# Optimization experiments

Hardware: AMD Instinct MI355X
Metric: run time of the kernel (lower is better)

## Reference

```python
import jax, jax.numpy as jnp
import numpy as np
import math

B, S, E, H = 2, 2048, 1024, 16
D = E // H  # head_dim = 64
WINDOW = 512
EPS = 1e-5


def _layernorm(x, gamma, beta):
    mu = jnp.mean(x, axis=-1, keepdims=True)
    var = jnp.var(x, axis=-1, keepdims=True)
    return (x - mu) * jax.lax.rsqrt(var + EPS) * gamma + beta


def setup_inputs() -> dict:
    key = jax.random.key(0)
    ks = jax.random.split(key, 5)
    return {
        "x": jax.random.normal(ks[0], (B, S, E), jnp.float32),
        "W_qkv": jax.random.normal(ks[1], (E, 3 * E), jnp.float32) * (E ** -0.5),
        "b_qkv": jax.random.normal(ks[2], (3 * E,), jnp.float32) * 0.02,
        "q_gamma": jnp.ones((D,), jnp.float32),
        "q_beta": jnp.zeros((D,), jnp.float32),
        "k_gamma": jnp.ones((D,), jnp.float32),
        "k_beta": jnp.zeros((D,), jnp.float32),
        "W_out": jax.random.normal(ks[3], (E, E), jnp.float32) * (E ** -0.5),
        "b_out": jax.random.normal(ks[4], (E,), jnp.float32) * 0.02,
    }


def reference(x, W_qkv, b_qkv, q_gamma, q_beta, k_gamma, k_beta, W_out, b_out):
    b, s, e = x.shape
    # fused QKV projection -> (3, B, H, S, D)
    qkv = (x @ W_qkv + b_qkv).reshape(b, s, 3, H, D).transpose(2, 0, 3, 1, 4)
    q, k, v = qkv[0], qkv[1], qkv[2]
    # qk_norm: LayerNorm over head_dim
    q = _layernorm(q, q_gamma, q_beta)
    k = _layernorm(k, k_gamma, k_beta)
    scores = jnp.einsum("bhqd,bhkd->bhqk", q, k) / math.sqrt(D)
    # causal + sliding-window mask (True = masked out)
    row = jnp.arange(s)[:, None]
    col = jnp.arange(s)[None, :]
    masked = (col > row) | (row - col >= WINDOW)  # sliding window subsumes causal
    scores = jnp.where(masked[None, None], -jnp.inf, scores)
    attn = jax.nn.softmax(scores, axis=-1)
    out = jnp.einsum("bhqk,bhkd->bhqd", attn, v)  # (B,H,S,D)
    out = out.transpose(0, 2, 1, 3).reshape(b, s, e)
    return out @ W_out + b_out
```

## Files before the change

### kernel.cpp

```cpp
#include <hip/hip_runtime.h>
#include <stdint.h>

typedef uint16_t u16;
typedef __attribute__((ext_vector_type(8))) short short8;
typedef __attribute__((ext_vector_type(4))) float f32x4;

#define DEV static __device__ __forceinline__

DEV u16 f2bf(float f) {
  uint32_t u = __float_as_uint(f);
  return (u16)((u + 0x7fffu + ((u >> 16) & 1u)) >> 16);
}
DEV float bf2f(u16 h) { return __uint_as_float(((uint32_t)h) << 16); }

DEV void gload16(const void* g, void* l) {
  __builtin_amdgcn_global_load_lds(
      (const __attribute__((address_space(1))) void*)g,
      (__attribute__((address_space(3))) void*)l, 16, 0, 0);
}

__global__ void k_cast4(const float* __restrict__ in, u16* __restrict__ out, int n4) {
  int i = blockIdx.x * blockDim.x + threadIdx.x;
  if (i >= n4) return;
  float4 v = ((const float4*)in)[i];
  uint2 p;
  p.x = (uint32_t)f2bf(v.x) | ((uint32_t)f2bf(v.y) << 16);
  p.y = (uint32_t)f2bf(v.z) | ((uint32_t)f2bf(v.w) << 16);
  ((uint2*)out)[i] = p;
}

__global__ void k_tcast(const float* __restrict__ Wm, u16* __restrict__ Wt, int K, int N) {
  __shared__ u16 t[64][65];
  int n0 = blockIdx.x * 64, k0 = blockIdx.y * 64;
  int tid = threadIdx.x;
#pragma unroll
  for (int i = 0; i < 16; ++i) {
    int idx = tid + i * 256, r = idx >> 6, c = idx & 63;
    t[r][c] = f2bf(Wm[(size_t)(k0 + r) * N + n0 + c]);
  }
  __syncthreads();
#pragma unroll
  for (int i = 0; i < 16; ++i) {
    int idx = tid + i * 256, r = idx >> 6, c = idx & 63;
    Wt[(size_t)(n0 + r) * K + k0 + c] = t[c][r];
  }
}

__global__ __launch_bounds__(256) void k_gemmqkv(
    const u16* __restrict__ A, const u16* __restrict__ Bt,
    const float* __restrict__ bias,
    const float* __restrict__ qg, const float* __restrict__ qb,
    const float* __restrict__ kg, const float* __restrict__ kb,
    u16* __restrict__ Qn, u16* __restrict__ Kn, u16* __restrict__ Vt) {
  const int K = 1024, N = 3072;
  __shared__ __attribute__((aligned(16))) u16 S[2][2][128 * 64];
  int bid = blockIdx.x;
  int ntn = N >> 7;
  int cpx = gridDim.x >> 3;
  int wg = (bid & 7) * cpx + (bid >> 3);
  int my = wg / ntn, nx = wg - my * ntn;
  int m0 = my * 128, n0 = nx * 128;
  int tid = threadIdx.x, lane = tid & 63, w = tid >> 6;
  int wr = (w >> 1) * 64, wc = (w & 1) * 64;
  int lr = lane & 15, lg = lane >> 4;
  int rsw = (lr & 7) << 3;
  int srow = tid >> 3;
  int scb = ((tid & 7) ^ ((tid >> 3) & 7)) * 8;
  f32x4 acc[4][4];
#pragma unroll
  for (int i = 0; i < 4; ++i)
#pragma unroll
    for (int j = 0; j < 4; ++j) acc[i][j] = (f32x4){0.f, 0.f, 0.f, 0.f};

  int nk = K >> 6;

#define STGQ(buf, kt)                                                                   \
  do {                                                                                  \
    gload16(A + (size_t)(m0 + srow) * K + (kt) * 64 + scb, &S[buf][0][tid * 8]);        \
    gload16(A + (size_t)(m0 + 32 + srow) * K + (kt) * 64 + scb, &S[buf][0][2048 + tid * 8]);  \
    gload16(A + (size_t)(m0 + 64 + srow) * K + (kt) * 64 + scb, &S[buf][0][4096 + tid * 8]);  \
    gload16(A + (size_t)(m0 + 96 + srow) * K + (kt) * 64 + scb, &S[buf][0][6144 + tid * 8]);  \
    gload16(Bt + (size_t)(n0 + srow) * K + (kt) * 64 + scb, &S[buf][1][tid * 8]);       \
    gload16(Bt + (size_t)(n0 + 32 + srow) * K + (kt) * 64 + scb, &S[buf][1][2048 + tid * 8]); \
    gload16(Bt + (size_t)(n0 + 64 + srow) * K + (kt) * 64 + scb, &S[buf][1][4096 + tid * 8]); \
    gload16(Bt + (size_t)(n0 + 96 + srow) * K + (kt) * 64 + scb, &S[buf][1][6144 + tid * 8]); \
  } while (0)

  STGQ(0, 0);
  asm volatile("s_waitcnt vmcnt(0)" ::: "memory");
  __syncthreads();

  for (int t = 0; t < nk; ++t) {
    int cur = t & 1;
    if (t + 1 < nk) STGQ(cur ^ 1, t + 1);
#pragma unroll
    for (int ks = 0; ks < 2; ++ks) {
      short8 af[4], bf[4];
#pragma unroll
      for (int mi = 0; mi < 4; ++mi)
        af[mi] = *(const short8*)&S[cur][0][((wr + mi * 16 + lr) * 64 + ks * 32 + lg * 8) ^ rsw];
#pragma unroll
      for (int ni = 0; ni < 4; ++ni)
        bf[ni] = *(const short8*)&S[cur][1][((wc + ni * 16 + lr) * 64 + ks * 32 + lg * 8) ^ rsw];
      __builtin_amdgcn_s_setprio(1);
#pragma unroll
      for (int mi = 0; mi < 4; ++mi)
#pragma unroll
        for (int ni = 0; ni < 4; ++ni)
          acc[mi][ni] = __builtin_amdgcn_mfma_f32_16x16x32_bf16(af[mi], bf[ni], acc[mi][ni], 0, 0, 0);
      __builtin_amdgcn_s_setprio(0);
    }
    asm volatile("s_waitcnt vmcnt(0)" ::: "memory");
    __syncthreads();
  }
#undef STGQ

  int rg = lg * 4;
  int sec = n0 >> 10;
  int hh = ((n0 + wc) >> 6) & 15;
  int b = m0 >> 11;
  int s0 = m0 & 2047;

  if (sec < 2) {
    const float* gp = sec ? kg : qg;
    const float* bp = sec ? kb : qb;
    float scl = sec ? 1.f : (0.125f * 1.44269504f);
    u16* op = sec ? Kn : Qn;
    float gv[4], bev[4], bb[4];
#pragma unroll
    for (int ni = 0; ni < 4; ++ni) {
      int d = ni * 16 + lr;
      gv[ni] = gp[d];
      bev[ni] = bp[d];
      bb[ni] = bias[n0 + wc + d];
    }
    size_t hb = (size_t)(b * 16 + hh) * 2048 * 64;
#pragma unroll
    for (int mi = 0; mi < 4; ++mi) {
      float a[4][4], ps[4], ps2[4];
#pragma unroll
      for (int ni = 0; ni < 4; ++ni)
#pragma unroll
        for (int j = 0; j < 4; ++j) a[ni][j] = acc[mi][ni][j] + bb[ni];
#pragma unroll
      for (int j = 0; j < 4; ++j) {
        ps[j] = a[0][j] + a[1][j] + a[2][j] + a[3][j];
        ps2[j] = a[0][j] * a[0][j] + a[1][j] * a[1][j] + a[2][j] * a[2][j] + a[3][j] * a[3][j];
      }
#pragma unroll
      for (int m = 1; m < 16; m <<= 1)
#pragma unroll
        for (int j = 0; j < 4; ++j) {
          ps[j] += __shfl_xor(ps[j], m, 64);
          ps2[j] += __shfl_xor(ps2[j], m, 64);
        }
#pragma unroll
      for (int j = 0; j < 4; ++j) {
        float mean = ps[j] * (1.f / 64);
        float var = ps2[j] * (1.f / 64) - mean * mean;
        float r = rsqrtf(var + 1e-5f);
        int row = s0 + wr + mi * 16 + rg + j;
        size_t base = hb + (size_t)row * 64;
#pragma unroll
        for (int ni = 0; ni < 4; ++ni) {
          float v = ((a[ni][j] - mean) * r * gv[ni] + bev[ni]) * scl;
          op[base + ni * 16 + lr] = f2bf(v);
        }
      }
    }
  } else {
    u16* vbase = Vt + (size_t)(b * 16 + hh) * 64 * 2048;
#pragma unroll
    for (int ni = 0; ni < 4; ++ni) {
      int d = ni * 16 + lr;
      float bb = bias[n0 + wc + d];
#pragma unroll
      for (int mi = 0; mi < 4; ++mi) {
        int row0 = s0 + wr + mi * 16 + rg;
        uint2 pk;
        pk.x = (uint32_t)f2bf(acc[mi][ni][0] + bb) | ((uint32_t)f2bf(acc[mi][ni][1] + bb) << 16);
        pk.y = (uint32_t)f2bf(acc[mi][ni][2] + bb) | ((uint32_t)f2bf(acc[mi][ni][3] + bb) << 16);
        *(uint2*)(vbase + (size_t)d * 2048 + row0) = pk;
      }
    }
  }
}

template <int OUT_BF16>
__global__ __launch_bounds__(256) void k_gemm4(
    const u16* __restrict__ A, const u16* __restrict__ Bt,
    const float* __restrict__ bias, void* __restrict__ Cout,
    int M, int N, int K) {
  __shared__ __attribute__((aligned(16))) u16 S[2][2][128 * 64];
  int bid = blockIdx.x;
  int ntn = N >> 7;
  int cpx = gridDim.x >> 3;
  int wg = (bid & 7) * cpx + (bid >> 3);
  int my = wg / ntn, nx = wg - my * ntn;
  int m0 = my * 128, n0 = nx * 128;
  int tid = threadIdx.x, lane = tid & 63, w = tid >> 6;
  int wr = (w >> 1) * 64, wc = (w & 1) * 64;
  int lr = lane & 15, lg = lane >> 4;
  int rsw = (lr & 7) << 3;
  int srow = tid >> 3;
  int scb = ((tid & 7) ^ ((tid >> 3) & 7)) * 8;
  f32x4 acc[4][4];
#pragma unroll
  for (int i = 0; i < 4; ++i)
#pragma unroll
    for (int j = 0; j < 4; ++j) acc[i][j] = (f32x4){0.f, 0.f, 0.f, 0.f};

  int nk = K >> 6;

#define STG4(buf, kt)                                                                   \
  do {                                                                                  \
    gload16(A + (size_t)(m0 + srow) * K + (kt) * 64 + scb, &S[buf][0][tid * 8]);        \
    gload16(A + (size_t)(m0 + 32 + srow) * K + (kt) * 64 + scb, &S[buf][0][2048 + tid * 8]);  \
    gload16(A + (size_t)(m0 + 64 + srow) * K + (kt) * 64 + scb, &S[buf][0][4096 + tid * 8]);  \
    gload16(A + (size_t)(m0 + 96 + srow) * K + (kt) * 64 + scb, &S[buf][0][6144 + tid * 8]);  \
    gload16(Bt + (size_t)(n0 + srow) * K + (kt) * 64 + scb, &S[buf][1][tid * 8]);       \
    gload16(Bt + (size_t)(n0 + 32 + srow) * K + (kt) * 64 + scb, &S[buf][1][2048 + tid * 8]); \
    gload16(Bt + (size_t)(n0 + 64 + srow) * K + (kt) * 64 + scb, &S[buf][1][4096 + tid * 8]); \
    gload16(Bt + (size_t)(n0 + 96 + srow) * K + (kt) * 64 + scb, &S[buf][1][6144 + tid * 8]); \
  } while (0)

  STG4(0, 0);
  asm volatile("s_waitcnt vmcnt(0)" ::: "memory");
  __syncthreads();

  for (int t = 0; t < nk; ++t) {
    int cur = t & 1;
    if (t + 1 < nk) STG4(cur ^ 1, t + 1);
#pragma unroll
    for (int ks = 0; ks < 2; ++ks) {
      short8 af[4], bf[4];
#pragma unroll
      for (int mi = 0; mi < 4; ++mi)
        af[mi] = *(const short8*)&S[cur][0][((wr + mi * 16 + lr) * 64 + ks * 32 + lg * 8) ^ rsw];
#pragma unroll
      for (int ni = 0; ni < 4; ++ni)
        bf[ni] = *(const short8*)&S[cur][1][((wc + ni * 16 + lr) * 64 + ks * 32 + lg * 8) ^ rsw];
      __builtin_amdgcn_s_setprio(1);
#pragma unroll
      for (int mi = 0; mi < 4; ++mi)
#pragma unroll
        for (int ni = 0; ni < 4; ++ni)
          acc[mi][ni] = __builtin_amdgcn_mfma_f32_16x16x32_bf16(af[mi], bf[ni], acc[mi][ni], 0, 0, 0);
      __builtin_amdgcn_s_setprio(0);
    }
    asm volatile("s_waitcnt vmcnt(0)" ::: "memory");
    __syncthreads();
  }
#undef STG4

  int rg = lg * 4;
#pragma unroll
  for (int mi = 0; mi < 4; ++mi) {
#pragma unroll
    for (int ni = 0; ni < 4; ++ni) {
      int col = n0 + wc + ni * 16 + lr;
      float bv = bias[col];
#pragma unroll
      for (int j = 0; j < 4; ++j) {
        int row = m0 + wr + mi * 16 + rg + j;
        float o = acc[mi][ni][j] + bv;
        if (OUT_BF16) ((u16*)Cout)[(size_t)row * N + col] = f2bf(o);
        else ((float*)Cout)[(size_t)row * N + col] = o;
      }
    }
  }
}

__global__ __launch_bounds__(256) void k_attn6(
    const u16* __restrict__ Qn, const u16* __restrict__ Kn,
    const u16* __restrict__ Vt, u16* __restrict__ attb) {
  __shared__ __attribute__((aligned(16))) u16 KL[2][4096];
  __shared__ __attribute__((aligned(16))) u16 VL[2][4096];
  __shared__ __attribute__((aligned(16))) u16 Pl[4][16 * 72];
  int bid = blockIdx.x;
  int xcd = bid & 7, idx = bid >> 3;
  int bh = xcd * 4 + (idx & 3);
  int qt = 31 - (idx >> 2);
  int q0 = qt * 64;
  int tid = threadIdx.x, lane = tid & 63, w = tid >> 6;
  int ln15 = lane & 15, lg = lane >> 4;
  int qlo = q0 + w * 16;
  const u16* Qh = Qn + (size_t)bh * (2048 * 64);
  const u16* Kh = Kn + (size_t)bh * (2048 * 64);
  const u16* Vh = Vt + (size_t)bh * (64 * 2048);
  int rsw = (ln15 & 7) << 3;
  int srow = tid >> 3;
  int scb = ((tid & 7) ^ ((tid >> 3) & 7)) * 8;

  short8 qf[2];
#pragma unroll
  for (int h2 = 0; h2 < 2; ++h2)
    qf[h2] = *(const short8*)(Qh + (size_t)(qlo + ln15) * 64 + h2 * 32 + lg * 8);

  f32x4 oacc[4];
#pragma unroll
  for (int dt = 0; dt < 4; ++dt) oacc[dt] = (f32x4){0.f, 0.f, 0.f, 0.f};
  float lwp[4] = {0.f, 0.f, 0.f, 0.f};

  int t0 = q0 >= 512 ? (q0 - 511) >> 6 : 0;
  int t1 = (q0 + 63) >> 6;

#define STAGE_A6(buf, kt)                                                              \
  do {                                                                                 \
    const u16* Kt_ = Kh + (size_t)(kt) * 4096;                                         \
    gload16(Kt_ + (size_t)srow * 64 + scb, &KL[buf][tid * 8]);                         \
    gload16(Kt_ + (size_t)(srow + 32) * 64 + scb, &KL[buf][2048 + tid * 8]);           \
    const u16* Vt_ = Vh + (size_t)(kt) * 64;                                           \
    gload16(Vt_ + (size_t)srow * 2048 + scb, &VL[buf][tid * 8]);                       \
    gload16(Vt_ + (size_t)(srow + 32) * 2048 + scb, &VL[buf][2048 + tid * 8]);         \
  } while (0)

  STAGE_A6(0, t0);
  asm volatile("s_waitcnt vmcnt(0)" ::: "memory");
  __syncthreads();

  for (int t = t0; t <= t1; ++t) {
    int cur = (t - t0) & 1;
    if (t + 1 <= t1) STAGE_A6(cur ^ 1, t + 1);
    int kt6 = t * 64;
    if (kt6 <= qlo + 15 && kt6 + 63 >= qlo - 511) {
      short8 kf[4][2];
#pragma unroll
      for (int c = 0; c < 4; ++c)
#pragma unroll
        for (int h2 = 0; h2 < 2; ++h2)
          kf[c][h2] = *(const short8*)&KL[cur][((c * 16 + ln15) * 64 + h2 * 32 + lg * 8) ^ rsw];
      f32x4 sf[4];
      __builtin_amdgcn_s_setprio(1);
#pragma unroll
      for (int c = 0; c < 4; ++c) {
        f32x4 z = (f32x4){0.f, 0.f, 0.f, 0.f};
        z = __builtin_amdgcn_mfma_f32_16x16x32_bf16(qf[0], kf[c][0], z, 0, 0, 0);
        sf[c] = __builtin_amdgcn_mfma_f32_16x16x32_bf16(qf[1], kf[c][1], z, 0, 0, 0);
      }
      __builtin_amdgcn_s_setprio(0);
      bool interior = (kt6 + 63 <= qlo) && (kt6 >= qlo - 496);
      if (interior) {
#pragma unroll
        for (int c = 0; c < 4; ++c)
#pragma unroll
          for (int j = 0; j < 4; ++j) {
            float p = __builtin_amdgcn_exp2f(sf[c][j]);
            sf[c][j] = p;
            lwp[j] += p;
          }
      } else {
#pragma unroll
        for (int c = 0; c < 4; ++c) {
          int kk = kt6 + c * 16 + ln15;
#pragma unroll
          for (int j = 0; j < 4; ++j) {
            int q = qlo + lg * 4 + j;
            bool msk = (kk > q) || ((q - kk) >= 512);
            float p = __builtin_amdgcn_exp2f(msk ? -1e30f : sf[c][j]);
            sf[c][j] = p;
            lwp[j] += p;
          }
        }
      }
#pragma unroll
      for (int c = 0; c < 4; ++c)
#pragma unroll
        for (int j = 0; j < 4; ++j) {
          uint32_t u = __float_as_uint(sf[c][j]);
          Pl[w][(lg * 4 + j) * 72 + c * 16 + ln15] = (u16)((u + 0x8000u) >> 16);
        }
      short8 vf[4][2];
#pragma unroll
      for (int dt = 0; dt < 4; ++dt)
#pragma unroll
        for (int h2 = 0; h2 < 2; ++h2)
          vf[dt][h2] = *(const short8*)&VL[cur][((dt * 16 + ln15) * 64 + h2 * 32 + lg * 8) ^ rsw];
      __builtin_amdgcn_s_setprio(1);
#pragma unroll
      for (int h2 = 0; h2 < 2; ++h2) {
        short8 pf = *(const short8*)&Pl[w][ln15 * 72 + h2 * 32 + lg * 8];
#pragma unroll
        for (int dt = 0; dt < 4; ++dt)
          oacc[dt] = __builtin_amdgcn_mfma_f32_16x16x32_bf16(pf, vf[dt][h2], oacc[dt], 0, 0, 0);
      }
      __builtin_amdgcn_s_setprio(0);
    }
    asm volatile("s_waitcnt vmcnt(0)" ::: "memory");
    __syncthreads();
  }
#undef STAGE_A6

  int b = bh >> 4, hh = bh & 15;
#pragma unroll
  for (int j = 0; j < 4; ++j) {
    float rs = lwp[j];
#pragma unroll
    for (int m = 8; m > 0; m >>= 1) rs += __shfl_xor(rs, m, 64);
    float inv = rs > 0.f ? 1.f / rs : 0.f;
    int row = b * 2048 + qlo + lg * 4 + j;
#pragma unroll
    for (int dt = 0; dt < 4; ++dt)
      attb[(size_t)row * 1024 + hh * 64 + dt * 16 + ln15] = f2bf(oacc[dt][j] * inv);
  }
}

extern "C" void kernel_launch(void* const* d_in, const int* in_sizes, int n_in,
                              void* d_out, int out_size, void* d_ws, size_t ws_size,
                              hipStream_t stream) {
  const float* x = (const float*)d_in[0];
  const float* Wqkv = (const float*)d_in[1];
  const float* bqkv = (const float*)d_in[2];
  const float* qg = (const float*)d_in[3];
  const float* qb = (const float*)d_in[4];
  const float* kg = (const float*)d_in[5];
  const float* kb = (const float*)d_in[6];
  const float* Wout = (const float*)d_in[7];
  const float* bout = (const float*)d_in[8];
  float* out = (float*)d_out;

  char* ws = (char*)d_ws;
  u16* attb = (u16*)(ws);
  u16* Vt = (u16*)(ws + 8388608);
  u16* Qn = (u16*)(ws + 16777216);
  u16* Kn = (u16*)(ws + 25165824);
  u16* xb = (u16*)(ws + 33554432);
  u16* wqkvT = (u16*)(ws + 41943040);
  u16* woutT = (u16*)(ws + 48234496);

  k_cast4<<<4096, 256, 0, stream>>>(x, xb, 4194304 / 4);
  k_tcast<<<dim3(48, 16), 256, 0, stream>>>(Wqkv, wqkvT, 1024, 3072);
  k_tcast<<<dim3(16, 16), 256, 0, stream>>>(Wout, woutT, 1024, 1024);
  k_gemmqkv<<<768, 256, 0, stream>>>(xb, wqkvT, bqkv, qg, qb, kg, kb, Qn, Kn, Vt);
  k_attn6<<<1024, 256, 0, stream>>>(Qn, Kn, Vt, attb);
  k_gemm4<0><<<256, 256, 0, stream>>>(attb, woutT, bout, out, 4096, 1024, 1024);
}
```

Before: 100.0 us.

## Double attention query tile per block to reuse staged K/V tiles

The attention kernel now handles 128 query rows per block (32 per wave, in two 16-row sub-tiles) instead of 64, and the grid is halved to 512 blocks. Each K/V tile staged in shared memory is reused across twice as many queries, which cuts global K/V traffic and staging overhead per query. The cost is more registers for the doubled accumulators, fewer blocks to fill the GPU, and more masked edge work because of the wider window span per block.

Result: no change. 99.74 us (-0.3%).

```diff
diff --git a/kernel.cpp b/kernel.cpp
--- a/kernel.cpp
+++ b/kernel.cpp
@@ -271,20 +271,20 @@
   }
 }
 
-__global__ __launch_bounds__(256) void k_attn6(
+__global__ __launch_bounds__(256) void k_attn7(
     const u16* __restrict__ Qn, const u16* __restrict__ Kn,
     const u16* __restrict__ Vt, u16* __restrict__ attb) {
   __shared__ __attribute__((aligned(16))) u16 KL[2][4096];
   __shared__ __attribute__((aligned(16))) u16 VL[2][4096];
-  __shared__ __attribute__((aligned(16))) u16 Pl[4][16 * 72];
+  __shared__ __attribute__((aligned(16))) u16 Pl[4][2304];
   int bid = blockIdx.x;
   int xcd = bid & 7, idx = bid >> 3;
   int bh = xcd * 4 + (idx & 3);
-  int qt = 31 - (idx >> 2);
-  int q0 = qt * 64;
+  int qb = 15 - (idx >> 2);
+  int q0 = qb * 128;
   int tid = threadIdx.x, lane = tid & 63, w = tid >> 6;
   int ln15 = lane & 15, lg = lane >> 4;
-  int qlo = q0 + w * 16;
+  int qlo = q0 + w * 32;
   const u16* Qh = Qn + (size_t)bh * (2048 * 64);
   const u16* Kh = Kn + (size_t)bh * (2048 * 64);
   const u16* Vh = Vt + (size_t)bh * (64 * 2048);
@@ -292,20 +292,28 @@
   int srow = tid >> 3;
   int scb = ((tid & 7) ^ ((tid >> 3) & 7)) * 8;
 
-  short8 qf[2];
-#pragma unroll
-  for (int h2 = 0; h2 < 2; ++h2)
-    qf[h2] = *(const short8*)(Qh + (size_t)(qlo + ln15) * 64 + h2 * 32 + lg * 8);
-
-  f32x4 oacc[4];
-#pragma unroll
-  for (int dt = 0; dt < 4; ++dt) oacc[dt] = (f32x4){0.f, 0.f, 0.f, 0.f};
-  float lwp[4] = {0.f, 0.f, 0.f, 0.f};
+  short8 qf[2][2];
+#pragma unroll
+  for (int qs = 0; qs < 2; ++qs)
+#pragma unroll
+    for (int h2 = 0; h2 < 2; ++h2)
+      qf[qs][h2] = *(const short8*)(Qh + (size_t)(qlo + qs * 16 + ln15) * 64 + h2 * 32 + lg * 8);
+
+  f32x4 oacc[2][4];
+#pragma unroll
+  for (int qs = 0; qs < 2; ++qs)
+#pragma unroll
+    for (int dt = 0; dt < 4; ++dt) oacc[qs][dt] = (f32x4){0.f, 0.f, 0.f, 0.f};
+  float lwp[2][4];
+#pragma unroll
+  for (int qs = 0; qs < 2; ++qs)
+#pragma unroll
+    for (int j = 0; j < 4; ++j) lwp[qs][j] = 0.f;
 
   int t0 = q0 >= 512 ? (q0 - 511) >> 6 : 0;
-  int t1 = (q0 + 63) >> 6;
-
-#define STAGE_A6(buf, kt)                                                              \
+  int t1 = (q0 + 127) >> 6;
+
+#define STAGE_A7(buf, kt)                                                              \
   do {                                                                                 \
     const u16* Kt_ = Kh + (size_t)(kt) * 4096;                                         \
     gload16(Kt_ + (size_t)srow * 64 + scb, &KL[buf][tid * 8]);                         \
@@ -315,61 +323,69 @@
     gload16(Vt_ + (size_t)(srow + 32) * 2048 + scb, &VL[buf][2048 + tid * 8]);         \
   } while (0)
 
-  STAGE_A6(0, t0);
+  STAGE_A7(0, t0);
   asm volatile("s_waitcnt vmcnt(0)" ::: "memory");
   __syncthreads();
 
   for (int t = t0; t <= t1; ++t) {
     int cur = (t - t0) & 1;
-    if (t + 1 <= t1) STAGE_A6(cur ^ 1, t + 1);
+    if (t + 1 <= t1) STAGE_A7(cur ^ 1, t + 1);
     int kt6 = t * 64;
-    if (kt6 <= qlo + 15 && kt6 + 63 >= qlo - 511) {
+    if (kt6 <= qlo + 31 && kt6 + 63 >= qlo - 511) {
       short8 kf[4][2];
 #pragma unroll
       for (int c = 0; c < 4; ++c)
 #pragma unroll
         for (int h2 = 0; h2 < 2; ++h2)
           kf[c][h2] = *(const short8*)&KL[cur][((c * 16 + ln15) * 64 + h2 * 32 + lg * 8) ^ rsw];
-      f32x4 sf[4];
+      f32x4 sf[2][4];
       __builtin_amdgcn_s_setprio(1);
 #pragma unroll
-      for (int c = 0; c < 4; ++c) {
-        f32x4 z = (f32x4){0.f, 0.f, 0.f, 0.f};
-        z = __builtin_amdgcn_mfma_f32_16x16x32_bf16(qf[0], kf[c][0], z, 0, 0, 0);
-        sf[c] = __builtin_amdgcn_mfma_f32_16x16x32_bf16(qf[1], kf[c][1], z, 0, 0, 0);
+      for (int qs = 0; qs < 2; ++qs)
+#pragma unroll
+        for (int c = 0; c < 4; ++c) {
+          f32x4 z = (f32x4){0.f, 0.f, 0.f, 0.f};
+          z = __builtin_amdgcn_mfma_f32_16x16x32_bf16(qf[qs][0], kf[c][0], z, 0, 0, 0);
+          sf[qs][c] = __builtin_amdgcn_mfma_f32_16x16x32_bf16(qf[qs][1], kf[c][1], z, 0, 0, 0);
+        }
+      __builtin_amdgcn_s_setprio(0);
+      bool interior = (kt6 + 63 <= qlo) && (kt6 >= qlo - 480);
+      if (interior) {
+#pragma unroll
+        for (int qs = 0; qs < 2; ++qs)
+#pragma unroll
+          for (int c = 0; c < 4; ++c)
+#pragma unroll
+            for (int j = 0; j < 4; ++j) {
+              float p = __builtin_amdgcn_exp2f(sf[qs][c][j]);
+              sf[qs][c][j] = p;
+              lwp[qs][j] += p;
+            }
+      } else {
+#pragma unroll
+        for (int qs = 0; qs < 2; ++qs)
+#pragma unroll
+          for (int c = 0; c < 4; ++c) {
+            int kk = kt6 + c * 16 + ln15;
+#pragma unroll
+            for (int j = 0; j < 4; ++j) {
+              int q = qlo + qs * 16 + lg * 4 + j;
+              bool msk = (kk > q) || ((q - kk) >= 512);
+              float p = __builtin_amdgcn_exp2f(msk ? -1e30f : sf[qs][c][j]);
+              sf[qs][c][j] = p;
+              lwp[qs][j] += p;
+            }
+          }
       }
-      __builtin_amdgcn_s_setprio(0);
-      bool interior = (kt6 + 63 <= qlo) && (kt6 >= qlo - 496);
-      if (interior) {
+#pragma unroll
+      for (int qs = 0; qs < 2; ++qs)
 #pragma unroll
         for (int c = 0; c < 4; ++c)
 #pragma unroll
           for (int j = 0; j < 4; ++j) {
-            float p = __builtin_amdgcn_exp2f(sf[c][j]);
-            sf[c][j] = p;
-            lwp[j] += p;
+            uint32_t u = __float_as_uint(sf[qs][c][j]);
+            Pl[w][(qs * 16 + lg * 4 + j) * 72 + c * 16 + ln15] = (u16)((u + 0x8000u) >> 16);
           }
-      } else {
-#pragma unroll
-        for (int c = 0; c < 4; ++c) {
-          int kk = kt6 + c * 16 + ln15;
-#pragma unroll
-          for (int j = 0; j < 4; ++j) {
-            int q = qlo + lg * 4 + j;
-            bool msk = (kk > q) || ((q - kk) >= 512);
-            float p = __builtin_amdgcn_exp2f(msk ? -1e30f : sf[c][j]);
-            sf[c][j] = p;
-            lwp[j] += p;
-          }
-        }
-      }
-#pragma unroll
-      for (int c = 0; c < 4; ++c)
-#pragma unroll
-        for (int j = 0; j < 4; ++j) {
-          uint32_t u = __float_as_uint(sf[c][j]);
-          Pl[w][(lg * 4 + j) * 72 + c * 16 + ln15] = (u16)((u + 0x8000u) >> 16);
-        }
       short8 vf[4][2];
 #pragma unroll
       for (int dt = 0; dt < 4; ++dt)
@@ -378,31 +394,35 @@
           vf[dt][h2] = *(const short8*)&VL[cur][((dt * 16 + ln15) * 64 + h2 * 32 + lg * 8) ^ rsw];
       __builtin_amdgcn_s_setprio(1);
 #pragma unroll
-      for (int h2 = 0; h2 < 2; ++h2) {
-        short8 pf = *(const short8*)&Pl[w][ln15 * 72 + h2 * 32 + lg * 8];
-#pragma unroll
-        for (int dt = 0; dt < 4; ++dt)
-          oacc[dt] = __builtin_amdgcn_mfma_f32_16x16x32_bf16(pf, vf[dt][h2], oacc[dt], 0, 0, 0);
-      }
+      for (int qs = 0; qs < 2; ++qs)
+#pragma unroll
+        for (int h2 = 0; h2 < 2; ++h2) {
+          short8 pf = *(const short8*)&Pl[w][(qs * 16 + ln15) * 72 + h2 * 32 + lg * 8];
+#pragma unroll
+          for (int dt = 0; dt < 4; ++dt)
+            oacc[qs][dt] = __builtin_amdgcn_mfma_f32_16x16x32_bf16(pf, vf[dt][h2], oacc[qs][dt], 0, 0, 0);
+        }
       __builtin_amdgcn_s_setprio(0);
     }
     asm volatile("s_waitcnt vmcnt(0)" ::: "memory");
     __syncthreads();
   }
-#undef STAGE_A6
+#undef STAGE_A7
 
   int b = bh >> 4, hh = bh & 15;
 #pragma unroll
-  for (int j = 0; j < 4; ++j) {
-    float rs = lwp[j];
-#pragma unroll
-    for (int m = 8; m > 0; m >>= 1) rs += __shfl_xor(rs, m, 64);
-    float inv = rs > 0.f ? 1.f / rs : 0.f;
-    int row = b * 2048 + qlo + lg * 4 + j;
-#pragma unroll
-    for (int dt = 0; dt < 4; ++dt)
-      attb[(size_t)row * 1024 + hh * 64 + dt * 16 + ln15] = f2bf(oacc[dt][j] * inv);
-  }
+  for (int qs = 0; qs < 2; ++qs)
+#pragma unroll
+    for (int j = 0; j < 4; ++j) {
+      float rs = lwp[qs][j];
+#pragma unroll
+      for (int m = 8; m > 0; m >>= 1) rs += __shfl_xor(rs, m, 64);
+      float inv = rs > 0.f ? 1.f / rs : 0.f;
+      int row = b * 2048 + qlo + qs * 16 + lg * 4 + j;
+#pragma unroll
+      for (int dt = 0; dt < 4; ++dt)
+        attb[(size_t)row * 1024 + hh * 64 + dt * 16 + ln15] = f2bf(oacc[qs][dt][j] * inv);
+    }
 }
 
 extern "C" void kernel_launch(void* const* d_in, const int* in_sizes, int n_in,
@@ -432,6 +452,6 @@
   k_tcast<<<dim3(48, 16), 256, 0, stream>>>(Wqkv, wqkvT, 1024, 3072);
   k_tcast<<<dim3(16, 16), 256, 0, stream>>>(Wout, woutT, 1024, 1024);
   k_gemmqkv<<<768, 256, 0, stream>>>(xb, wqkvT, bqkv, qg, qb, kg, kb, Qn, Kn, Vt);
-  k_attn6<<<1024, 256, 0, stream>>>(Qn, Kn, Vt, attb);
+  k_attn7<<<512, 256, 0, stream>>>(Qn, Kn, Vt, attb);
   k_gemm4<0><<<256, 256, 0, stream>>>(attb, woutT, bout, out, 4096, 1024, 1024);
 }
```
